# Optimization experiments

Hardware: AMD Instinct MI355X
Metric: run time of the kernel (lower is better)

Reference implementation:

```python
import jax, jax.numpy as jnp
import numpy as np

EPS = 1e-8


def setup_inputs() -> dict:
    key = jax.random.key(0)
    ks = jax.random.split(key, 6)
    N, H, B = 1000000, 256, 1024
    x = jax.random.normal(ks[0], (N, H), dtype=jnp.float32)
    W1 = jax.random.normal(ks[1], (H, H // 2), dtype=jnp.float32) * (1.0 / np.sqrt(H))
    b1 = jax.random.normal(ks[2], (H // 2,), dtype=jnp.float32) * 0.01
    W2 = jax.random.normal(ks[3], (H // 2, 1), dtype=jnp.float32) * (1.0 / np.sqrt(H // 2))
    b2 = jax.random.normal(ks[4], (1,), dtype=jnp.float32) * 0.01
    batch = jnp.sort(jax.random.randint(ks[5], (N,), 0, B, dtype=jnp.int64))
    return {"x": x, "W1": W1, "b1": b1, "W2": W2, "b2": b2,
            "batch": batch, "batch_size": B}


def reference(x, W1, b1, W2, b2, batch, batch_size):
    # attention MLP: Linear -> Tanh -> Linear -> softmax over all nodes (dim 0)
    scores = jnp.tanh(x @ W1 + b1) @ W2 + b2          # [N, 1]
    w = jax.nn.softmax(scores, axis=0)[:, 0]           # [N]
    # per-graph normalization (segment sums replace the dense one-hot mask)
    seg_sum = jax.ops.segment_sum(w, batch, num_segments=batch_size)  # [B]
    w_norm = w / (seg_sum[batch] + EPS)                # [N]
    # weighted per-graph feature aggregation
    graph_embedding = jax.ops.segment_sum(w_norm[:, None] * x, batch,
                                          num_segments=batch_size)   # [B, H]
    return graph_embedding
```

## Files before the change

### kernel.cpp

```cpp
#include <hip/hip_runtime.h>
#include <hip/hip_bf16.h>
#include <cstdint>


#define H_DIM 256
#define HID   128
#define CHUNK 64
#define XT_STRIDE 264

typedef _Float16 half8 __attribute__((ext_vector_type(8)));
typedef _Float16 half4 __attribute__((ext_vector_type(4)));
typedef float floatx4 __attribute__((ext_vector_type(4)));

__device__ __forceinline__ float fast_tanh(float y) {
    float e2 = __expf(2.0f * y);
    return 1.0f - 2.0f / (e2 + 1.0f);
}

__global__ void prep_w1(const float* __restrict__ W1, _Float16* __restrict__ w1h) {
    int idx = blockIdx.x * blockDim.x + threadIdx.x;
    if (idx >= 8 * 8 * 64 * 8) return;
    int j  = idx & 7;
    int l  = (idx >> 3) & 63;
    int ks = (idx >> 9) & 7;
    int nt = idx >> 12;
    int k = ks * 32 + ((l >> 4) << 3) + j;
    int n = nt * 16 + (l & 15);
    w1h[idx] = (_Float16)W1[k * HID + n];
}

__global__ __launch_bounds__(256, 4) void fused_kernel(
    const float* __restrict__ x, const _Float16* __restrict__ w1h,
    const float* __restrict__ b1, const float* __restrict__ W2,
    const float* __restrict__ b2, const int* __restrict__ batch,
    float* __restrict__ out, int N)
{
    __shared__ __align__(16) _Float16 xt[CHUNK * XT_STRIDE];
    __shared__ float pbuf[4][CHUNK];
    __shared__ float wbuf[CHUNK];
    __shared__ float fz[2];

    int tid = threadIdx.x, b = blockIdx.x;
    int wave = tid >> 6, lane = tid & 63, g = lane >> 4, c = lane & 15;
    int colg = tid & 31, rowg = tid >> 5;

    int lo = 0, hi = N;
    while (lo < hi) { int mid = (lo + hi) >> 1; if (batch[mid] < b) lo = mid + 1; else hi = mid; }
    int start = lo; hi = N;
    while (lo < hi) { int mid = (lo + hi) >> 1; if (batch[mid] <= b) lo = mid + 1; else hi = mid; }
    int end = lo;
    int seglen = end - start;
    if (seglen <= 0) { out[(size_t)b * H_DIM + tid] = 0.0f; return; }

    float b1r[2], w2r[2];
#pragma unroll
    for (int nt2 = 0; nt2 < 2; ++nt2) {
        b1r[nt2] = b1[(2 * wave + nt2) * 16 + c];
        w2r[nt2] = W2[(2 * wave + nt2) * 16 + c];
    }
    float b2v = b2[0];

    float m_run = -3.0e38f;
    float Zrun  = 0.0f;
    float a[8];
#pragma unroll
    for (int k2 = 0; k2 < 8; ++k2) a[k2] = 0.0f;

    for (int co = 0; co < seglen; co += CHUNK) {
        int cnt = min(CHUNK, seglen - co);

        __syncthreads();

#pragma unroll
        for (int bb = 0; bb < 4; ++bb) {
            float4 rv[4];
#pragma unroll
            for (int i = 0; i < 4; ++i) {
                int fi = tid + (bb * 4 + i) * 256;
                int row = fi >> 6, col4 = fi & 63;
                int rr = row < cnt ? row : cnt - 1;
                rv[i] = *(const float4*)(x + (size_t)(start + co + rr) * H_DIM + col4 * 4);
            }
#pragma unroll
            for (int i = 0; i < 4; ++i) {
                int fi = tid + (bb * 4 + i) * 256;
                int row = fi >> 6, col4 = fi & 63;
                half4 hv;
                hv[0] = (_Float16)rv[i].x; hv[1] = (_Float16)rv[i].y;
                hv[2] = (_Float16)rv[i].z; hv[3] = (_Float16)rv[i].w;
                *(half4*)&xt[row * XT_STRIDE + col4 * 4] = hv;
            }
        }

        __syncthreads();

        floatx4 acc[4][2];
#pragma unroll
        for (int mt = 0; mt < 4; ++mt)
#pragma unroll
            for (int nt2 = 0; nt2 < 2; ++nt2)
#pragma unroll
                for (int q = 0; q < 4; ++q) acc[mt][nt2][q] = 0.0f;

        const half8* bbase = (const half8*)&w1h[((2 * wave * 8) * 64 + lane) * 8];
#pragma unroll
        for (int ks = 0; ks < 8; ++ks) {
            half8 bf0 = bbase[ks * 64];
            half8 bf1 = bbase[(8 + ks) * 64];
#pragma unroll
            for (int mt = 0; mt < 4; ++mt) {
                half8 af = *(const half8*)&xt[(mt * 16 + c) * XT_STRIDE + ks * 32 + g * 8];
                acc[mt][0] = __builtin_amdgcn_mfma_f32_16x16x32_f16(af, bf0, acc[mt][0], 0, 0, 0);
                acc[mt][1] = __builtin_amdgcn_mfma_f32_16x16x32_f16(af, bf1, acc[mt][1], 0, 0, 0);
            }
        }

#pragma unroll
        for (int mt = 0; mt < 4; ++mt) {
#pragma unroll
            for (int r = 0; r < 4; ++r) {
                float p = fast_tanh(acc[mt][0][r] + b1r[0]) * w2r[0]
                        + fast_tanh(acc[mt][1][r] + b1r[1]) * w2r[1];
                p += __shfl_xor(p, 8);
                p += __shfl_xor(p, 4);
                p += __shfl_xor(p, 2);
                p += __shfl_xor(p, 1);
                if (c == 0) pbuf[wave][mt * 16 + g * 4 + r] = p;
            }
        }

        __syncthreads();

        if (wave == 0) {
            float sv = (lane < cnt)
                ? (pbuf[0][lane] + pbuf[1][lane] + pbuf[2][lane] + pbuf[3][lane] + b2v)
                : -3.0e38f;
            float cm = sv;
#pragma unroll
            for (int off = 32; off; off >>= 1) cm = fmaxf(cm, __shfl_xor(cm, off));
            float m_new = fmaxf(m_run, cm);
            float f = __expf(m_run - m_new);
            float w = __expf(sv - m_new);
            wbuf[lane] = w;
            float sw = w;
#pragma unroll
            for (int off = 32; off; off >>= 1) sw += __shfl_xor(sw, off);
            Zrun = Zrun * f + sw;
            m_run = m_new;
            if (lane == 0) fz[0] = f;
        }

        __syncthreads();

        float f = fz[0];
#pragma unroll
        for (int k2 = 0; k2 < 8; ++k2) a[k2] *= f;
#pragma unroll
        for (int i = 0; i < 8; ++i) {
            int j = rowg + 8 * i;
            float w = wbuf[j];
            half8 hx = *(const half8*)&xt[j * XT_STRIDE + colg * 8];
#pragma unroll
            for (int k2 = 0; k2 < 8; ++k2)
                a[k2] = fmaf((float)hx[k2], w, a[k2]);
        }
    }

    if (tid == 0) fz[1] = Zrun;

    __syncthreads();
    float* scr = (float*)xt;
    *(float4*)&scr[rowg * 256 + colg * 8]     = make_float4(a[0], a[1], a[2], a[3]);
    *(float4*)&scr[rowg * 256 + colg * 8 + 4] = make_float4(a[4], a[5], a[6], a[7]);
    __syncthreads();
    float r = 0.0f;
#pragma unroll
    for (int i = 0; i < 8; ++i) r += scr[i * 256 + tid];
    out[(size_t)b * H_DIM + tid] = r / fz[1];
}

extern "C" void kernel_launch(void* const* d_in, const int* in_sizes, int n_in,
                              void* d_out, int out_size, void* d_ws, size_t ws_size,
                              hipStream_t stream) {
    const float* x    = (const float*)d_in[0];
    const float* W1   = (const float*)d_in[1];
    const float* b1   = (const float*)d_in[2];
    const float* W2   = (const float*)d_in[3];
    const float* b2   = (const float*)d_in[4];
    const int*   batch = (const int*)d_in[5];
    int N = in_sizes[5];
    int B = out_size / H_DIM;

    _Float16* w1h = (_Float16*)d_ws;

    prep_w1<<<32768 / 256, 256, 0, stream>>>(W1, w1h);
    fused_kernel<<<B, 256, 0, stream>>>(x, w1h, b1, W2, b2, batch, (float*)d_out, N);
}
```

Before: 398.7 us.

## Double-buffer x chunks in LDS with register prefetch of the next chunk

Halves the chunk size to 32 rows and adds a second LDS buffer. The global loads for chunk t+1 are issued into registers before chunk t is converted and processed, so HBM latency overlaps with the MFMA, softmax and aggregation work. This also drops one barrier per chunk. In exchange, each thread holds 16 float4 prefetch registers, which may cut occupancy, and the smaller chunks mean more barriers and online-softmax steps per segment.

Result: slower. 592.4 us (+48.6%).

```diff
diff --git a/kernel.cpp b/kernel.cpp
--- a/kernel.cpp
+++ b/kernel.cpp
@@ -5,7 +5,7 @@
 
 #define H_DIM 256
 #define HID   128
-#define CHUNK 64
+#define CHUNK 32
 #define XT_STRIDE 264
 
 typedef _Float16 half8 __attribute__((ext_vector_type(8)));
@@ -35,7 +35,7 @@
     const float* __restrict__ b2, const int* __restrict__ batch,
     float* __restrict__ out, int N)
 {
-    __shared__ __align__(16) _Float16 xt[CHUNK * XT_STRIDE];
+    __shared__ __align__(16) _Float16 xt[2][CHUNK * XT_STRIDE];
     __shared__ float pbuf[4][CHUNK];
     __shared__ float wbuf[CHUNK];
     __shared__ float fz[2];
@@ -51,6 +51,7 @@
     int end = lo;
     int seglen = end - start;
     if (seglen <= 0) { out[(size_t)b * H_DIM + tid] = 0.0f; return; }
+    int nch = (seglen + CHUNK - 1) / CHUNK;
 
     float b1r[2], w2r[2];
 #pragma unroll
@@ -66,37 +67,37 @@
 #pragma unroll
     for (int k2 = 0; k2 < 8; ++k2) a[k2] = 0.0f;
 
-    for (int co = 0; co < seglen; co += CHUNK) {
-        int cnt = min(CHUNK, seglen - co);
-
+    auto load_chunk = [&](float4 (&r)[8], int t) {
+        int base = start + t * CHUNK;
+        int cnt = end - base; if (cnt > CHUNK) cnt = CHUNK;
+#pragma unroll
+        for (int i = 0; i < 8; ++i) {
+            int fi = tid + i * 256;
+            int row = fi >> 6, col4 = fi & 63;
+            int rr = row < cnt ? row : cnt - 1;
+            r[i] = *(const float4*)(x + (size_t)(base + rr) * H_DIM + col4 * 4);
+        }
+    };
+
+    auto step = [&](float4 (&cur)[8], float4 (&nxt)[8], int t, _Float16* xb) {
+        int cnt = seglen - t * CHUNK; if (cnt > CHUNK) cnt = CHUNK;
+
+        if (t + 1 < nch) load_chunk(nxt, t + 1);
+
+#pragma unroll
+        for (int i = 0; i < 8; ++i) {
+            int fi = tid + i * 256;
+            int row = fi >> 6, col4 = fi & 63;
+            half4 hv;
+            hv[0] = (_Float16)cur[i].x; hv[1] = (_Float16)cur[i].y;
+            hv[2] = (_Float16)cur[i].z; hv[3] = (_Float16)cur[i].w;
+            *(half4*)&xb[row * XT_STRIDE + col4 * 4] = hv;
+        }
         __syncthreads();
 
-#pragma unroll
-        for (int bb = 0; bb < 4; ++bb) {
-            float4 rv[4];
-#pragma unroll
-            for (int i = 0; i < 4; ++i) {
-                int fi = tid + (bb * 4 + i) * 256;
-                int row = fi >> 6, col4 = fi & 63;
-                int rr = row < cnt ? row : cnt - 1;
-                rv[i] = *(const float4*)(x + (size_t)(start + co + rr) * H_DIM + col4 * 4);
-            }
-#pragma unroll
-            for (int i = 0; i < 4; ++i) {
-                int fi = tid + (bb * 4 + i) * 256;
-                int row = fi >> 6, col4 = fi & 63;
-                half4 hv;
-                hv[0] = (_Float16)rv[i].x; hv[1] = (_Float16)rv[i].y;
-                hv[2] = (_Float16)rv[i].z; hv[3] = (_Float16)rv[i].w;
-                *(half4*)&xt[row * XT_STRIDE + col4 * 4] = hv;
-            }
-        }
-
-        __syncthreads();
-
-        floatx4 acc[4][2];
-#pragma unroll
-        for (int mt = 0; mt < 4; ++mt)
+        floatx4 acc[2][2];
+#pragma unroll
+        for (int mt = 0; mt < 2; ++mt)
 #pragma unroll
             for (int nt2 = 0; nt2 < 2; ++nt2)
 #pragma unroll
@@ -108,15 +109,15 @@
             half8 bf0 = bbase[ks * 64];
             half8 bf1 = bbase[(8 + ks) * 64];
 #pragma unroll
-            for (int mt = 0; mt < 4; ++mt) {
-                half8 af = *(const half8*)&xt[(mt * 16 + c) * XT_STRIDE + ks * 32 + g * 8];
+            for (int mt = 0; mt < 2; ++mt) {
+                half8 af = *(const half8*)&xb[(mt * 16 + c) * XT_STRIDE + ks * 32 + g * 8];
                 acc[mt][0] = __builtin_amdgcn_mfma_f32_16x16x32_f16(af, bf0, acc[mt][0], 0, 0, 0);
                 acc[mt][1] = __builtin_amdgcn_mfma_f32_16x16x32_f16(af, bf1, acc[mt][1], 0, 0, 0);
             }
         }
 
 #pragma unroll
-        for (int mt = 0; mt < 4; ++mt) {
+        for (int mt = 0; mt < 2; ++mt) {
 #pragma unroll
             for (int r = 0; r < 4; ++r) {
                 float p = fast_tanh(acc[mt][0][r] + b1r[0]) * w2r[0]
@@ -128,7 +129,6 @@
                 if (c == 0) pbuf[wave][mt * 16 + g * 4 + r] = p;
             }
         }
-
         __syncthreads();
 
         if (wave == 0) {
@@ -137,39 +137,45 @@
                 : -3.0e38f;
             float cm = sv;
 #pragma unroll
-            for (int off = 32; off; off >>= 1) cm = fmaxf(cm, __shfl_xor(cm, off));
+            for (int off = 16; off; off >>= 1) cm = fmaxf(cm, __shfl_xor(cm, off));
             float m_new = fmaxf(m_run, cm);
             float f = __expf(m_run - m_new);
             float w = __expf(sv - m_new);
-            wbuf[lane] = w;
+            if (lane < CHUNK) wbuf[lane] = w;
             float sw = w;
 #pragma unroll
-            for (int off = 32; off; off >>= 1) sw += __shfl_xor(sw, off);
+            for (int off = 16; off; off >>= 1) sw += __shfl_xor(sw, off);
             Zrun = Zrun * f + sw;
             m_run = m_new;
             if (lane == 0) fz[0] = f;
         }
-
         __syncthreads();
 
         float f = fz[0];
 #pragma unroll
         for (int k2 = 0; k2 < 8; ++k2) a[k2] *= f;
 #pragma unroll
-        for (int i = 0; i < 8; ++i) {
+        for (int i = 0; i < 4; ++i) {
             int j = rowg + 8 * i;
             float w = wbuf[j];
-            half8 hx = *(const half8*)&xt[j * XT_STRIDE + colg * 8];
+            half8 hx = *(const half8*)&xb[j * XT_STRIDE + colg * 8];
 #pragma unroll
             for (int k2 = 0; k2 < 8; ++k2)
                 a[k2] = fmaf((float)hx[k2], w, a[k2]);
         }
+    };
+
+    float4 rg[8], rn[8];
+    load_chunk(rg, 0);
+    for (int t = 0; t < nch; t += 2) {
+        step(rg, rn, t, xt[0]);
+        if (t + 1 < nch) step(rn, rg, t + 1, xt[1]);
     }
 
     if (tid == 0) fz[1] = Zrun;
 
     __syncthreads();
-    float* scr = (float*)xt;
+    float* scr = (float*)&xt[0][0];
     *(float4*)&scr[rowg * 256 + colg * 8]     = make_float4(a[0], a[1], a[2], a[3]);
     *(float4*)&scr[rowg * 256 + colg * 8 + 4] = make_float4(a[4], a[5], a[6], a[7]);
     __syncthreads();
```

## Split each segment across two blocks with a softmax-merge combine kernel

Applied to the files above, without the earlier changes.

Each graph segment is now processed by two blocks, each covering half its rows and writing a partial max, partial normalizer and partial weighted sum to workspace. A new combine kernel merges the two partials with online-softmax rescaling. The chunk size drops to 32 rows to cut shared memory and allow more resident blocks, and x is read with nontemporal 32-byte loads. The aim is better latency hiding and fuller use of the GPU's CUs when only 1024 segments exist, at the cost of an extra launch and more per-chunk synchronization.

Result: slower. 500.5 us (+25.5%).

```diff
diff --git a/kernel.cpp b/kernel.cpp
--- a/kernel.cpp
+++ b/kernel.cpp
@@ -5,12 +5,12 @@
 
 #define H_DIM 256
 #define HID   128
-#define CHUNK 64
+#define CHUNK 32
 #define XT_STRIDE 264
 
 typedef _Float16 half8 __attribute__((ext_vector_type(8)));
-typedef _Float16 half4 __attribute__((ext_vector_type(4)));
 typedef float floatx4 __attribute__((ext_vector_type(4)));
+typedef float fvec4 __attribute__((ext_vector_type(4)));
 
 __device__ __forceinline__ float fast_tanh(float y) {
     float e2 = __expf(2.0f * y);
@@ -29,18 +29,20 @@
     w1h[idx] = (_Float16)W1[k * HID + n];
 }
 
-__global__ __launch_bounds__(256, 4) void fused_kernel(
+__global__ __launch_bounds__(256, 8) void fused_kernel(
     const float* __restrict__ x, const _Float16* __restrict__ w1h,
     const float* __restrict__ b1, const float* __restrict__ W2,
     const float* __restrict__ b2, const int* __restrict__ batch,
-    float* __restrict__ out, int N)
+    float* __restrict__ pm, float* __restrict__ pz, float* __restrict__ pacc,
+    int N)
 {
     __shared__ __align__(16) _Float16 xt[CHUNK * XT_STRIDE];
     __shared__ float pbuf[4][CHUNK];
     __shared__ float wbuf[CHUNK];
     __shared__ float fz[2];
 
-    int tid = threadIdx.x, b = blockIdx.x;
+    int tid = threadIdx.x, blk = blockIdx.x;
+    int b = blk >> 1, sub = blk & 1;
     int wave = tid >> 6, lane = tid & 63, g = lane >> 4, c = lane & 15;
     int colg = tid & 31, rowg = tid >> 5;
 
@@ -50,7 +52,16 @@
     while (lo < hi) { int mid = (lo + hi) >> 1; if (batch[mid] <= b) lo = mid + 1; else hi = mid; }
     int end = lo;
     int seglen = end - start;
-    if (seglen <= 0) { out[(size_t)b * H_DIM + tid] = 0.0f; return; }
+    int h = (seglen + 1) >> 1;
+    int sstart = start + sub * h;
+    int send = sub ? end : start + h;
+    int sslen = send - sstart;
+
+    if (sslen <= 0) {
+        pacc[(size_t)blk * H_DIM + tid] = 0.0f;
+        if (tid == 0) { pm[blk] = -3.0e38f; pz[blk] = 0.0f; }
+        return;
+    }
 
     float b1r[2], w2r[2];
 #pragma unroll
@@ -66,37 +77,32 @@
 #pragma unroll
     for (int k2 = 0; k2 < 8; ++k2) a[k2] = 0.0f;
 
-    for (int co = 0; co < seglen; co += CHUNK) {
-        int cnt = min(CHUNK, seglen - co);
-
-        __syncthreads();
-
-#pragma unroll
-        for (int bb = 0; bb < 4; ++bb) {
-            float4 rv[4];
-#pragma unroll
-            for (int i = 0; i < 4; ++i) {
-                int fi = tid + (bb * 4 + i) * 256;
-                int row = fi >> 6, col4 = fi & 63;
-                int rr = row < cnt ? row : cnt - 1;
-                rv[i] = *(const float4*)(x + (size_t)(start + co + rr) * H_DIM + col4 * 4);
-            }
-#pragma unroll
-            for (int i = 0; i < 4; ++i) {
-                int fi = tid + (bb * 4 + i) * 256;
-                int row = fi >> 6, col4 = fi & 63;
-                half4 hv;
-                hv[0] = (_Float16)rv[i].x; hv[1] = (_Float16)rv[i].y;
-                hv[2] = (_Float16)rv[i].z; hv[3] = (_Float16)rv[i].w;
-                *(half4*)&xt[row * XT_STRIDE + col4 * 4] = hv;
-            }
-        }
-
-        __syncthreads();
-
-        floatx4 acc[4][2];
-#pragma unroll
-        for (int mt = 0; mt < 4; ++mt)
+    for (int co = 0; co < sslen; co += CHUNK) {
+        int cnt = sslen - co; if (cnt > CHUNK) cnt = CHUNK;
+
+        __syncthreads();
+
+#pragma unroll
+        for (int i = 0; i < 4; ++i) {
+            int p = tid + i * 256;
+            int row = p >> 5, col8 = p & 31;
+            int rr = row < cnt ? row : cnt - 1;
+            const fvec4* sp = (const fvec4*)(x + (size_t)(sstart + co + rr) * H_DIM + col8 * 8);
+            fvec4 v0 = __builtin_nontemporal_load(sp);
+            fvec4 v1 = __builtin_nontemporal_load(sp + 1);
+            half8 hv;
+            hv[0] = (_Float16)v0.x; hv[1] = (_Float16)v0.y;
+            hv[2] = (_Float16)v0.z; hv[3] = (_Float16)v0.w;
+            hv[4] = (_Float16)v1.x; hv[5] = (_Float16)v1.y;
+            hv[6] = (_Float16)v1.z; hv[7] = (_Float16)v1.w;
+            *(half8*)&xt[row * XT_STRIDE + col8 * 8] = hv;
+        }
+
+        __syncthreads();
+
+        floatx4 acc[2][2];
+#pragma unroll
+        for (int mt = 0; mt < 2; ++mt)
 #pragma unroll
             for (int nt2 = 0; nt2 < 2; ++nt2)
 #pragma unroll
@@ -108,7 +114,7 @@
             half8 bf0 = bbase[ks * 64];
             half8 bf1 = bbase[(8 + ks) * 64];
 #pragma unroll
-            for (int mt = 0; mt < 4; ++mt) {
+            for (int mt = 0; mt < 2; ++mt) {
                 half8 af = *(const half8*)&xt[(mt * 16 + c) * XT_STRIDE + ks * 32 + g * 8];
                 acc[mt][0] = __builtin_amdgcn_mfma_f32_16x16x32_f16(af, bf0, acc[mt][0], 0, 0, 0);
                 acc[mt][1] = __builtin_amdgcn_mfma_f32_16x16x32_f16(af, bf1, acc[mt][1], 0, 0, 0);
@@ -116,7 +122,7 @@
         }
 
 #pragma unroll
-        for (int mt = 0; mt < 4; ++mt) {
+        for (int mt = 0; mt < 2; ++mt) {
 #pragma unroll
             for (int r = 0; r < 4; ++r) {
                 float p = fast_tanh(acc[mt][0][r] + b1r[0]) * w2r[0]
@@ -128,35 +134,33 @@
                 if (c == 0) pbuf[wave][mt * 16 + g * 4 + r] = p;
             }
         }
-
-        __syncthreads();
-
-        if (wave == 0) {
+        __syncthreads();
+
+        if (wave == 0 && lane < CHUNK) {
             float sv = (lane < cnt)
                 ? (pbuf[0][lane] + pbuf[1][lane] + pbuf[2][lane] + pbuf[3][lane] + b2v)
                 : -3.0e38f;
             float cm = sv;
 #pragma unroll
-            for (int off = 32; off; off >>= 1) cm = fmaxf(cm, __shfl_xor(cm, off));
+            for (int off = 16; off; off >>= 1) cm = fmaxf(cm, __shfl_xor(cm, off));
             float m_new = fmaxf(m_run, cm);
             float f = __expf(m_run - m_new);
             float w = __expf(sv - m_new);
             wbuf[lane] = w;
             float sw = w;
 #pragma unroll
-            for (int off = 32; off; off >>= 1) sw += __shfl_xor(sw, off);
+            for (int off = 16; off; off >>= 1) sw += __shfl_xor(sw, off);
             Zrun = Zrun * f + sw;
             m_run = m_new;
             if (lane == 0) fz[0] = f;
         }
-
         __syncthreads();
 
         float f = fz[0];
 #pragma unroll
         for (int k2 = 0; k2 < 8; ++k2) a[k2] *= f;
 #pragma unroll
-        for (int i = 0; i < 8; ++i) {
+        for (int i = 0; i < 4; ++i) {
             int j = rowg + 8 * i;
             float w = wbuf[j];
             half8 hx = *(const half8*)&xt[j * XT_STRIDE + colg * 8];
@@ -165,8 +169,6 @@
                 a[k2] = fmaf((float)hx[k2], w, a[k2]);
         }
     }
-
-    if (tid == 0) fz[1] = Zrun;
 
     __syncthreads();
     float* scr = (float*)xt;
@@ -176,7 +178,24 @@
     float r = 0.0f;
 #pragma unroll
     for (int i = 0; i < 8; ++i) r += scr[i * 256 + tid];
-    out[(size_t)b * H_DIM + tid] = r / fz[1];
+    pacc[(size_t)blk * H_DIM + tid] = r;
+    if (tid == 0) { pm[blk] = m_run; pz[blk] = Zrun; }
+}
+
+__global__ __launch_bounds__(256) void combine_kernel(
+    const float* __restrict__ pm, const float* __restrict__ pz,
+    const float* __restrict__ pacc, float* __restrict__ out)
+{
+    int b = blockIdx.x, tid = threadIdx.x;
+    float m0 = pm[2 * b], m1 = pm[2 * b + 1];
+    float Z0 = pz[2 * b], Z1 = pz[2 * b + 1];
+    float m = fmaxf(m0, m1);
+    float f0 = Z0 > 0.0f ? __expf(m0 - m) : 0.0f;
+    float f1 = Z1 > 0.0f ? __expf(m1 - m) : 0.0f;
+    float Z = f0 * Z0 + f1 * Z1;
+    float num = f0 * pacc[(size_t)(2 * b) * H_DIM + tid]
+              + f1 * pacc[(size_t)(2 * b + 1) * H_DIM + tid];
+    out[(size_t)b * H_DIM + tid] = Z > 0.0f ? num / Z : 0.0f;
 }
 
 extern "C" void kernel_launch(void* const* d_in, const int* in_sizes, int n_in,
@@ -190,9 +209,14 @@
     const int*   batch = (const int*)d_in[5];
     int N = in_sizes[5];
     int B = out_size / H_DIM;
+    int nsub = 2 * B;
 
     _Float16* w1h = (_Float16*)d_ws;
+    float* pm   = (float*)((char*)d_ws + 65536);
+    float* pz   = pm + nsub;
+    float* pacc = pz + nsub;
 
     prep_w1<<<32768 / 256, 256, 0, stream>>>(W1, w1h);
-    fused_kernel<<<B, 256, 0, stream>>>(x, w1h, b1, W2, b2, batch, (float*)d_out, N);
-}
+    fused_kernel<<<nsub, 256, 0, stream>>>(x, w1h, b1, W2, b2, batch, pm, pz, pacc, N);
+    combine_kernel<<<B, 256, 0, stream>>>(pm, pz, pacc, (float*)d_out);
+}
```
